# Performance work log

Hardware: AMD Instinct MI355X
Metric: run time of the kernel (lower is better)

The kernel has to match this reference:

```python
import jax, jax.numpy as jnp
import numpy as np

B, C, H, W = 16, 64, 64, 64
C1, C2 = 8, 32  # block_channels_1 = C/8, block_channels_2 = C/2


def _conv1x1(x, w, b):
    # x: [B,C,H,W], w: [O,C] (1x1 kernel), b: [O]
    return jnp.einsum('bchw,oc->bohw', x, w) + b[None, :, None, None]


def _maxpool2(x):
    # MaxPool2d(kernel_size=2): window 2x2, stride 2, no padding
    return jax.lax.reduce_window(x, -jnp.inf, jax.lax.max,
                                 (1, 1, 2, 2), (1, 1, 2, 2), 'VALID')


def setup_inputs() -> dict:
    key = jax.random.key(0)
    ks = jax.random.split(key, 10)
    s = lambda fan_in: 1.0 / np.sqrt(fan_in)
    return {
        'nonlocal_input': jax.random.normal(ks[0], (B, C, H, W), jnp.float32),
        # spectral-normalized conv weights are treated as the effective (already
        # normalized) weights; 1x1 kernels stored as [out, in]
        'w_delta': jax.random.normal(ks[1], (C1, C), jnp.float32) * s(C),
        'b_delta': jax.random.normal(ks[2], (C1,), jnp.float32) * 0.01,
        'w_phi': jax.random.normal(ks[3], (C1, C), jnp.float32) * s(C),
        'b_phi': jax.random.normal(ks[4], (C1,), jnp.float32) * 0.01,
        'w_g': jax.random.normal(ks[5], (C2, C), jnp.float32) * s(C),
        'b_g': jax.random.normal(ks[6], (C2,), jnp.float32) * 0.01,
        'w_last': jax.random.normal(ks[7], (C, C2), jnp.float32) * s(C2),
        'b_last': jax.random.normal(ks[8], (C,), jnp.float32) * 0.01,
        # torch init is zeros; use a nonzero value so the attention path matters
        'gamma': jnp.asarray([0.7], jnp.float32),
    }


def reference(nonlocal_input, w_delta, b_delta, w_phi, b_phi, w_g, b_g,
              w_last, b_last, gamma):
    x = nonlocal_input
    b, c, h, w = x.shape

    # delta: [B,C1,H,W] -> [B, HW, C1]
    delta = _conv1x1(x, w_delta, b_delta)
    delta = jnp.transpose(delta, (0, 2, 3, 1)).reshape(b, h * w, C1)

    # phi: conv + pool -> [B,C1,H/2,W/2]; NOTE: the original permutes
    # (1,0,2,3) BEFORE reshaping to [B, C1, HW/4] (faithful to source).
    phi = _maxpool2(_conv1x1(x, w_phi, b_phi))
    phi = jnp.transpose(phi, (1, 0, 2, 3)).reshape(b, C1, -1)

    # attention: [B, HW, HW/4]
    attn = jax.nn.softmax(jnp.einsum('bnk,bkm->bnm', delta, phi), axis=-1)

    # g: conv + pool -> [B, HW/4, C2]
    g = _maxpool2(_conv1x1(x, w_g, b_g))
    g = jnp.transpose(g, (0, 2, 3, 1)).reshape(b, -1, C2)

    out = jnp.einsum('bnm,bmc->bnc', attn, g)          # [B, HW, C2]
    out = out.reshape(b, h, w, C2).transpose(0, 3, 1, 2)  # [B, C2, H, W]

    return gamma[0] * _conv1x1(out, w_last, b_last) + x
```

## Files before the change

### kernel.cpp

```cpp
#include <hip/hip_runtime.h>
#include <hip/hip_bf16.h>
#include <math.h>

typedef __attribute__((ext_vector_type(8))) short bf16x8;
typedef __attribute__((ext_vector_type(4))) float f32x4;

#define B_   16
#define C_   64
#define C1_  8
#define C2_  32
#define HW_  4096
#define M_   1024
#define LOG2E 1.4426950408889634f
#define MFMA_BF16 __builtin_amdgcn_mfma_f32_16x16x32_bf16

__device__ __forceinline__ unsigned short f2bf(float f) {
  union { float f; unsigned u; } v; v.f = f;
  unsigned r = (v.u + 0x7fffu + ((v.u >> 16) & 1u)) >> 16;
  return (unsigned short)r;
}
__device__ __forceinline__ float bf2f(unsigned short h) {
  union { unsigned u; float f; } v; v.u = ((unsigned)h) << 16;
  return v.f;
}

__global__ __launch_bounds__(256, 4)
void k_pre(const float* __restrict__ x,
           const float* __restrict__ w_delta, const float* __restrict__ b_delta,
           const float* __restrict__ w_phi,  const float* __restrict__ b_phi,
           const float* __restrict__ w_g,    const float* __restrict__ b_g,
           unsigned short* __restrict__ delta_s,
           unsigned short* __restrict__ phi_s,
           unsigned short* __restrict__ g_t) {
  __shared__ float wd_s[C_*C1_];
  __shared__ float wp_s[C_*C1_];
  __shared__ float wg_s[C_*C2_];
  __shared__ float comb[2*64*49];
  int tid = threadIdx.x;
  for (int i = tid; i < C1_*C_; i += 256) {
    int o = i >> 6, c = i & 63;
    wd_s[c*C1_ + o] = w_delta[i];
    wp_s[c*C1_ + o] = w_phi[i];
  }
  for (int i = tid; i < C2_*C_; i += 256) {
    int o = i >> 6, c = i & 63;
    wg_s[c*C2_ + o] = w_g[i];
  }
  __syncthreads();

  int qt  = tid >> 6;
  int sub = tid & 63;
  int id  = blockIdx.x * 64 + sub;
  int pix = id & 3;
  int pm  = id >> 2;
  int b = pm >> 10;
  int m = pm & 1023;
  int py = 2*(m >> 5) + (pix >> 1);
  int px = 2*(m & 31) + (pix & 1);
  int n = py * 64 + px;

  const float* xp = x + ((size_t)b*C_ + qt*16)*HW_ + n;
  float xv[16];
  #pragma unroll
  for (int i = 0; i < 16; ++i) xv[i] = xp[(size_t)i * HW_];

  float ad[8], ap[8], ag[32];
  #pragma unroll
  for (int o = 0; o < 8; ++o) { ad[o] = 0.f; ap[o] = 0.f; }
  #pragma unroll
  for (int o = 0; o < 32; ++o) ag[o] = 0.f;

  int c0 = qt * 16;
  #pragma unroll
  for (int i = 0; i < 16; ++i) {
    int c = c0 + i;
    float v = xv[i];
    #pragma unroll
    for (int t = 0; t < 2; ++t) {
      float4 w = ((const float4*)(wd_s + c*C1_))[t];
      ad[4*t+0] += v*w.x; ad[4*t+1] += v*w.y; ad[4*t+2] += v*w.z; ad[4*t+3] += v*w.w;
    }
    #pragma unroll
    for (int t = 0; t < 2; ++t) {
      float4 w = ((const float4*)(wp_s + c*C1_))[t];
      ap[4*t+0] += v*w.x; ap[4*t+1] += v*w.y; ap[4*t+2] += v*w.z; ap[4*t+3] += v*w.w;
    }
    #pragma unroll
    for (int t = 0; t < 8; ++t) {
      float4 w = ((const float4*)(wg_s + c*C2_))[t];
      ag[4*t+0] += v*w.x; ag[4*t+1] += v*w.y; ag[4*t+2] += v*w.z; ag[4*t+3] += v*w.w;
    }
  }

  if (qt == 1 || qt == 3) {
    float* cb = comb + (((qt >> 1)*64) + sub)*49;
    #pragma unroll
    for (int o = 0; o < 8; ++o) { cb[o] = ad[o]; cb[8+o] = ap[o]; }
    #pragma unroll
    for (int o = 0; o < 32; ++o) cb[16+o] = ag[o];
  }
  __syncthreads();
  if (qt == 0 || qt == 2) {
    const float* cb = comb + (((qt >> 1)*64) + sub)*49;
    #pragma unroll
    for (int o = 0; o < 8; ++o) { ad[o] += cb[o]; ap[o] += cb[8+o]; }
    #pragma unroll
    for (int o = 0; o < 32; ++o) ag[o] += cb[16+o];
  }
  __syncthreads();
  if (qt == 2) {
    float* cb = comb + sub*49;
    #pragma unroll
    for (int o = 0; o < 8; ++o) { cb[o] = ad[o]; cb[8+o] = ap[o]; }
    #pragma unroll
    for (int o = 0; o < 32; ++o) cb[16+o] = ag[o];
  }
  __syncthreads();
  if (qt == 0) {
    const float* cb = comb + sub*49;
    #pragma unroll
    for (int o = 0; o < 8; ++o) { ad[o] += cb[o]; ap[o] += cb[8+o]; }
    #pragma unroll
    for (int o = 0; o < 32; ++o) ag[o] += cb[16+o];

    __align__(16) unsigned short row[16];
    #pragma unroll
    for (int o = 0; o < 8; ++o) {
      float v = (ad[o] + b_delta[o]) * LOG2E;
      unsigned short hi = f2bf(v);
      row[o]   = hi;
      row[8+o] = f2bf(v - bf2f(hi));
    }
    uint4* dst = (uint4*)(delta_s + ((size_t)b*HW_ + n)*16);
    dst[0] = *(uint4*)&row[0];
    dst[1] = *(uint4*)&row[8];

    #pragma unroll
    for (int o = 0; o < 8; ++o) {
      float v = ap[o];
      v = fmaxf(v, __shfl_xor(v, 1));
      v = fmaxf(v, __shfl_xor(v, 2));
      ap[o] = v;
    }
    #pragma unroll
    for (int o = 0; o < 32; ++o) {
      float v = ag[o];
      v = fmaxf(v, __shfl_xor(v, 1));
      v = fmaxf(v, __shfl_xor(v, 2));
      ag[o] = v;
    }

    if ((sub & 3) == 0) {
      #pragma unroll
      for (int cp = 0; cp < 8; ++cp) {
        int f = cp*16 + b;
        float v = ap[cp] + b_phi[cp];
        unsigned short hi = f2bf(v);
        unsigned short* pr = phi_s + ((size_t)(f >> 3)*M_ + m)*16;
        pr[f & 7]       = hi;
        pr[8 + (f & 7)] = f2bf(v - bf2f(hi));
      }
      #pragma unroll
      for (int o = 0; o < 32; ++o)
        g_t[((size_t)b*C2_ + o)*M_ + m] = f2bf(ag[o] + b_g[o]);
    }
  }
}

__global__ __launch_bounds__(256, 4)
void k_attn(const float* __restrict__ x,
            const unsigned short* __restrict__ delta_s,
            const unsigned short* __restrict__ phi_s,
            const unsigned short* __restrict__ g_t,
            const float* __restrict__ w_last,
            const float* __restrict__ b_last,
            const float* __restrict__ gamma,
            float* __restrict__ out) {
  __shared__ float cmb[2*32*40];
  __shared__ float o_sh[64*33];
  int tid  = threadIdx.x;
  int lane = tid & 63;
  int wv   = tid >> 6;
  int rg   = wv & 1;
  int kh   = wv >> 1;
  int r    = lane & 15;
  int q    = lane >> 4;
  int bx = blockIdx.x;
  int b  = bx >> 6;
  int n0 = (bx & 63) * 64;
  int row0 = n0 + rg*32;

  bf16x8 dfrag0 = *(const bf16x8*)(delta_s + ((size_t)b*HW_ + row0 + r)*16      + (q & 1)*8);
  bf16x8 dfrag1 = *(const bf16x8*)(delta_s + ((size_t)b*HW_ + row0 + 16 + r)*16 + (q & 1)*8);

  const unsigned short* phib = phi_s + (size_t)b*M_*16;
  const unsigned short* gb0  = g_t + ((size_t)b*C2_ + r)      * M_;
  const unsigned short* gb1  = g_t + ((size_t)b*C2_ + 16 + r) * M_;
  int phi_off = (q >> 1) * 8;
  int key0 = (r >> 2)*8 + (r & 3);
  int key1 = key0 + 4;

  bf16x8 ones;
  #pragma unroll
  for (int i = 0; i < 8; ++i) ones[i] = (short)0x3F80;

  f32x4 acc00 = {0,0,0,0}, acc01 = {0,0,0,0};
  f32x4 acc10 = {0,0,0,0}, acc11 = {0,0,0,0};
  f32x4 accd0 = {0,0,0,0}, accd1 = {0,0,0,0};
  f32x4 zero  = {0,0,0,0};

  int kbase = kh * 512;
  #pragma unroll 4
  for (int kc = 0; kc < 512; kc += 32) {
    int k0 = kbase + kc;
    bf16x8 aphi0 = *(const bf16x8*)(phib + (size_t)(k0 + key0)*16 + phi_off);
    bf16x8 aphi1 = *(const bf16x8*)(phib + (size_t)(k0 + key1)*16 + phi_off);
    bf16x8 bg0   = *(const bf16x8*)(gb0 + k0 + q*8);
    bf16x8 bg1   = *(const bf16x8*)(gb1 + k0 + q*8);

    f32x4 s0 = MFMA_BF16(aphi0, dfrag0, zero, 0, 0, 0);
    f32x4 s1 = MFMA_BF16(aphi1, dfrag0, zero, 0, 0, 0);
    union { bf16x8 v; __hip_bfloat162 h[4]; } e0;
    e0.h[0] = __float22bfloat162_rn(make_float2(__builtin_amdgcn_exp2f(s0[0]),
                                                __builtin_amdgcn_exp2f(s0[1])));
    e0.h[1] = __float22bfloat162_rn(make_float2(__builtin_amdgcn_exp2f(s0[2]),
                                                __builtin_amdgcn_exp2f(s0[3])));
    e0.h[2] = __float22bfloat162_rn(make_float2(__builtin_amdgcn_exp2f(s1[0]),
                                                __builtin_amdgcn_exp2f(s1[1])));
    e0.h[3] = __float22bfloat162_rn(make_float2(__builtin_amdgcn_exp2f(s1[2]),
                                                __builtin_amdgcn_exp2f(s1[3])));
    acc00 = MFMA_BF16(e0.v, bg0, acc00, 0, 0, 0);
    acc01 = MFMA_BF16(e0.v, bg1, acc01, 0, 0, 0);
    accd0 = MFMA_BF16(e0.v, ones, accd0, 0, 0, 0);

    f32x4 t0 = MFMA_BF16(aphi0, dfrag1, zero, 0, 0, 0);
    f32x4 t1 = MFMA_BF16(aphi1, dfrag1, zero, 0, 0, 0);
    union { bf16x8 v; __hip_bfloat162 h[4]; } e1;
    e1.h[0] = __float22bfloat162_rn(make_float2(__builtin_amdgcn_exp2f(t0[0]),
                                                __builtin_amdgcn_exp2f(t0[1])));
    e1.h[1] = __float22bfloat162_rn(make_float2(__builtin_amdgcn_exp2f(t0[2]),
                                                __builtin_amdgcn_exp2f(t0[3])));
    e1.h[2] = __float22bfloat162_rn(make_float2(__builtin_amdgcn_exp2f(t1[0]),
                                                __builtin_amdgcn_exp2f(t1[1])));
    e1.h[3] = __float22bfloat162_rn(make_float2(__builtin_amdgcn_exp2f(t1[2]),
                                                __builtin_amdgcn_exp2f(t1[3])));
    acc10 = MFMA_BF16(e1.v, bg0, acc10, 0, 0, 0);
    acc11 = MFMA_BF16(e1.v, bg1, acc11, 0, 0, 0);
    accd1 = MFMA_BF16(e1.v, ones, accd1, 0, 0, 0);
  }

  if (kh == 1) {
    float* cb = cmb + rg*32*40;
    #pragma unroll
    for (int reg = 0; reg < 4; ++reg) {
      int lr = q*4 + reg;
      cb[lr*40 + r]           = acc00[reg];
      cb[lr*40 + 16 + r]      = acc01[reg];
      cb[(16+lr)*40 + r]      = acc10[reg];
      cb[(16+lr)*40 + 16 + r] = acc11[reg];
      if (r == 0) {
        cb[lr*40 + 32]      = accd0[reg];
        cb[(16+lr)*40 + 32] = accd1[reg];
      }
    }
  }
  __syncthreads();
  if (kh == 0) {
    const float* cb = cmb + rg*32*40;
    #pragma unroll
    for (int reg = 0; reg < 4; ++reg) {
      int lr = q*4 + reg;
      float den0 = accd0[reg] + cb[lr*40 + 32];
      float den1 = accd1[reg] + cb[(16+lr)*40 + 32];
      float i0 = __builtin_amdgcn_rcpf(den0);
      float i1 = __builtin_amdgcn_rcpf(den1);
      o_sh[(rg*32 + lr)*33 + r]           = (acc00[reg] + cb[lr*40 + r])           * i0;
      o_sh[(rg*32 + lr)*33 + 16 + r]      = (acc01[reg] + cb[lr*40 + 16 + r])      * i0;
      o_sh[(rg*32 + 16 + lr)*33 + r]      = (acc10[reg] + cb[(16+lr)*40 + r])      * i1;
      o_sh[(rg*32 + 16 + lr)*33 + 16 + r] = (acc11[reg] + cb[(16+lr)*40 + 16 + r]) * i1;
    }
  }
  __syncthreads();

  int rr = tid & 63;
  int wq = tid >> 6;
  float o_reg[32];
  #pragma unroll
  for (int c = 0; c < 32; ++c) o_reg[c] = o_sh[rr*33 + c];
  float gm = gamma[0];
  for (int i = 0; i < 16; ++i) {
    int co = wq*16 + i;
    float a = b_last[co];
    #pragma unroll
    for (int c = 0; c < 32; ++c) a += w_last[co*32 + c] * o_reg[c];
    size_t oi = ((size_t)b*C_ + co)*HW_ + (size_t)(n0 + rr);
    out[oi] = gm * a + x[oi];
  }
}

extern "C" void kernel_launch(void* const* d_in, const int* in_sizes, int n_in,
                              void* d_out, int out_size, void* d_ws, size_t ws_size,
                              hipStream_t stream) {
  const float* x       = (const float*)d_in[0];
  const float* w_delta = (const float*)d_in[1];
  const float* b_delta = (const float*)d_in[2];
  const float* w_phi   = (const float*)d_in[3];
  const float* b_phi   = (const float*)d_in[4];
  const float* w_g     = (const float*)d_in[5];
  const float* b_g     = (const float*)d_in[6];
  const float* w_last  = (const float*)d_in[7];
  const float* b_last  = (const float*)d_in[8];
  const float* gamma   = (const float*)d_in[9];
  float* out = (float*)d_out;

  unsigned short* ws = (unsigned short*)d_ws;
  unsigned short* delta_s = ws;
  unsigned short* phi_s   = ws + (size_t)B_*HW_*16;
  unsigned short* g_t     = phi_s + (size_t)B_*M_*16;

  hipLaunchKernelGGL(k_pre, dim3(1024), dim3(256), 0, stream,
                     x, w_delta, b_delta, w_phi, b_phi, w_g, b_g,
                     delta_s, phi_s, g_t);
  hipLaunchKernelGGL(k_attn, dim3(1024), dim3(256), 0, stream,
                     x, delta_s, phi_s, g_t, w_last, b_last, gamma, out);
}
```

Before: 135.1 us.

## Split attention keys four ways per block and drop shared weight staging in pre kernel

The attention kernel now has each of its four waves cover all 64 query rows over a quarter of the key range. Previously waves were split two-by-two over row groups and key halves. This lets each loaded phi and g fragment feed four row tiles instead of two, cutting global load traffic per MFMA, at the cost of more accumulator registers and a three-way LDS reduction. The pre kernel also stops staging conv weights in shared memory with a barrier and reads them directly from global memory, relying on cache and scalar loads.

```diff
diff --git a/kernel.cpp b/kernel.cpp
--- a/kernel.cpp
+++ b/kernel.cpp
@@ -32,21 +32,8 @@
            unsigned short* __restrict__ delta_s,
            unsigned short* __restrict__ phi_s,
            unsigned short* __restrict__ g_t) {
-  __shared__ float wd_s[C_*C1_];
-  __shared__ float wp_s[C_*C1_];
-  __shared__ float wg_s[C_*C2_];
   __shared__ float comb[2*64*49];
   int tid = threadIdx.x;
-  for (int i = tid; i < C1_*C_; i += 256) {
-    int o = i >> 6, c = i & 63;
-    wd_s[c*C1_ + o] = w_delta[i];
-    wp_s[c*C1_ + o] = w_phi[i];
-  }
-  for (int i = tid; i < C2_*C_; i += 256) {
-    int o = i >> 6, c = i & 63;
-    wg_s[c*C2_ + o] = w_g[i];
-  }
-  __syncthreads();
 
   int qt  = tid >> 6;
   int sub = tid & 63;
@@ -59,37 +46,29 @@
   int px = 2*(m & 31) + (pix & 1);
   int n = py * 64 + px;
 
-  const float* xp = x + ((size_t)b*C_ + qt*16)*HW_ + n;
+  int c0 = qt * 16;
+  const float* xp = x + ((size_t)b*C_ + c0)*HW_ + n;
   float xv[16];
   #pragma unroll
   for (int i = 0; i < 16; ++i) xv[i] = xp[(size_t)i * HW_];
 
   float ad[8], ap[8], ag[32];
   #pragma unroll
-  for (int o = 0; o < 8; ++o) { ad[o] = 0.f; ap[o] = 0.f; }
-  #pragma unroll
-  for (int o = 0; o < 32; ++o) ag[o] = 0.f;
-
-  int c0 = qt * 16;
-  #pragma unroll
-  for (int i = 0; i < 16; ++i) {
-    int c = c0 + i;
-    float v = xv[i];
-    #pragma unroll
-    for (int t = 0; t < 2; ++t) {
-      float4 w = ((const float4*)(wd_s + c*C1_))[t];
-      ad[4*t+0] += v*w.x; ad[4*t+1] += v*w.y; ad[4*t+2] += v*w.z; ad[4*t+3] += v*w.w;
-    }
-    #pragma unroll
-    for (int t = 0; t < 2; ++t) {
-      float4 w = ((const float4*)(wp_s + c*C1_))[t];
-      ap[4*t+0] += v*w.x; ap[4*t+1] += v*w.y; ap[4*t+2] += v*w.z; ap[4*t+3] += v*w.w;
-    }
-    #pragma unroll
-    for (int t = 0; t < 8; ++t) {
-      float4 w = ((const float4*)(wg_s + c*C2_))[t];
-      ag[4*t+0] += v*w.x; ag[4*t+1] += v*w.y; ag[4*t+2] += v*w.z; ag[4*t+3] += v*w.w;
-    }
+  for (int o = 0; o < 8; ++o) {
+    const float* wd = w_delta + o*C_ + c0;
+    const float* wp = w_phi   + o*C_ + c0;
+    float accd = 0.f, accp = 0.f;
+    #pragma unroll
+    for (int i = 0; i < 16; ++i) { accd += xv[i]*wd[i]; accp += xv[i]*wp[i]; }
+    ad[o] = accd; ap[o] = accp;
+  }
+  #pragma unroll
+  for (int o = 0; o < 32; ++o) {
+    const float* wg = w_g + o*C_ + c0;
+    float a = 0.f;
+    #pragma unroll
+    for (int i = 0; i < 16; ++i) a += xv[i]*wg[i];
+    ag[o] = a;
   }
 
   if (qt == 1 || qt == 3) {
@@ -176,22 +155,21 @@
             const float* __restrict__ b_last,
             const float* __restrict__ gamma,
             float* __restrict__ out) {
-  __shared__ float cmb[2*32*40];
+  __shared__ float cmb[3*64*37];
   __shared__ float o_sh[64*33];
   int tid  = threadIdx.x;
   int lane = tid & 63;
-  int wv   = tid >> 6;
-  int rg   = wv & 1;
-  int kh   = wv >> 1;
+  int kh   = tid >> 6;
   int r    = lane & 15;
   int q    = lane >> 4;
   int bx = blockIdx.x;
   int b  = bx >> 6;
   int n0 = (bx & 63) * 64;
-  int row0 = n0 + rg*32;
-
-  bf16x8 dfrag0 = *(const bf16x8*)(delta_s + ((size_t)b*HW_ + row0 + r)*16      + (q & 1)*8);
-  bf16x8 dfrag1 = *(const bf16x8*)(delta_s + ((size_t)b*HW_ + row0 + 16 + r)*16 + (q & 1)*8);
+
+  bf16x8 df[4];
+  #pragma unroll
+  for (int t = 0; t < 4; ++t)
+    df[t] = *(const bf16x8*)(delta_s + ((size_t)b*HW_ + n0 + t*16 + r)*16 + (q & 1)*8);
 
   const unsigned short* phib = phi_s + (size_t)b*M_*16;
   const unsigned short* gb0  = g_t + ((size_t)b*C2_ + r)      * M_;
@@ -204,80 +182,74 @@
   #pragma unroll
   for (int i = 0; i < 8; ++i) ones[i] = (short)0x3F80;
 
-  f32x4 acc00 = {0,0,0,0}, acc01 = {0,0,0,0};
-  f32x4 acc10 = {0,0,0,0}, acc11 = {0,0,0,0};
-  f32x4 accd0 = {0,0,0,0}, accd1 = {0,0,0,0};
-  f32x4 zero  = {0,0,0,0};
-
-  int kbase = kh * 512;
-  #pragma unroll 4
-  for (int kc = 0; kc < 512; kc += 32) {
+  f32x4 acc[4][2];
+  f32x4 den[4];
+  f32x4 zero = {0,0,0,0};
+  #pragma unroll
+  for (int t = 0; t < 4; ++t) { acc[t][0] = zero; acc[t][1] = zero; den[t] = zero; }
+
+  int kbase = kh * 256;
+  #pragma unroll 2
+  for (int kc = 0; kc < 256; kc += 32) {
     int k0 = kbase + kc;
     bf16x8 aphi0 = *(const bf16x8*)(phib + (size_t)(k0 + key0)*16 + phi_off);
     bf16x8 aphi1 = *(const bf16x8*)(phib + (size_t)(k0 + key1)*16 + phi_off);
     bf16x8 bg0   = *(const bf16x8*)(gb0 + k0 + q*8);
     bf16x8 bg1   = *(const bf16x8*)(gb1 + k0 + q*8);
 
-    f32x4 s0 = MFMA_BF16(aphi0, dfrag0, zero, 0, 0, 0);
-    f32x4 s1 = MFMA_BF16(aphi1, dfrag0, zero, 0, 0, 0);
-    union { bf16x8 v; __hip_bfloat162 h[4]; } e0;
-    e0.h[0] = __float22bfloat162_rn(make_float2(__builtin_amdgcn_exp2f(s0[0]),
-                                                __builtin_amdgcn_exp2f(s0[1])));
-    e0.h[1] = __float22bfloat162_rn(make_float2(__builtin_amdgcn_exp2f(s0[2]),
-                                                __builtin_amdgcn_exp2f(s0[3])));
-    e0.h[2] = __float22bfloat162_rn(make_float2(__builtin_amdgcn_exp2f(s1[0]),
-                                                __builtin_amdgcn_exp2f(s1[1])));
-    e0.h[3] = __float22bfloat162_rn(make_float2(__builtin_amdgcn_exp2f(s1[2]),
-                                                __builtin_amdgcn_exp2f(s1[3])));
-    acc00 = MFMA_BF16(e0.v, bg0, acc00, 0, 0, 0);
-    acc01 = MFMA_BF16(e0.v, bg1, acc01, 0, 0, 0);
-    accd0 = MFMA_BF16(e0.v, ones, accd0, 0, 0, 0);
-
-    f32x4 t0 = MFMA_BF16(aphi0, dfrag1, zero, 0, 0, 0);
-    f32x4 t1 = MFMA_BF16(aphi1, dfrag1, zero, 0, 0, 0);
-    union { bf16x8 v; __hip_bfloat162 h[4]; } e1;
-    e1.h[0] = __float22bfloat162_rn(make_float2(__builtin_amdgcn_exp2f(t0[0]),
-                                                __builtin_amdgcn_exp2f(t0[1])));
-    e1.h[1] = __float22bfloat162_rn(make_float2(__builtin_amdgcn_exp2f(t0[2]),
-                                                __builtin_amdgcn_exp2f(t0[3])));
-    e1.h[2] = __float22bfloat162_rn(make_float2(__builtin_amdgcn_exp2f(t1[0]),
-                                                __builtin_amdgcn_exp2f(t1[1])));
-    e1.h[3] = __float22bfloat162_rn(make_float2(__builtin_amdgcn_exp2f(t1[2]),
-                                                __builtin_amdgcn_exp2f(t1[3])));
-    acc10 = MFMA_BF16(e1.v, bg0, acc10, 0, 0, 0);
-    acc11 = MFMA_BF16(e1.v, bg1, acc11, 0, 0, 0);
-    accd1 = MFMA_BF16(e1.v, ones, accd1, 0, 0, 0);
-  }
-
-  if (kh == 1) {
-    float* cb = cmb + rg*32*40;
-    #pragma unroll
-    for (int reg = 0; reg < 4; ++reg) {
-      int lr = q*4 + reg;
-      cb[lr*40 + r]           = acc00[reg];
-      cb[lr*40 + 16 + r]      = acc01[reg];
-      cb[(16+lr)*40 + r]      = acc10[reg];
-      cb[(16+lr)*40 + 16 + r] = acc11[reg];
-      if (r == 0) {
-        cb[lr*40 + 32]      = accd0[reg];
-        cb[(16+lr)*40 + 32] = accd1[reg];
+    #pragma unroll
+    for (int t = 0; t < 4; ++t) {
+      f32x4 s0 = MFMA_BF16(aphi0, df[t], zero, 0, 0, 0);
+      f32x4 s1 = MFMA_BF16(aphi1, df[t], zero, 0, 0, 0);
+      union { bf16x8 v; __hip_bfloat162 h[4]; } e;
+      e.h[0] = __float22bfloat162_rn(make_float2(__builtin_amdgcn_exp2f(s0[0]),
+                                                 __builtin_amdgcn_exp2f(s0[1])));
+      e.h[1] = __float22bfloat162_rn(make_float2(__builtin_amdgcn_exp2f(s0[2]),
+                                                 __builtin_amdgcn_exp2f(s0[3])));
+      e.h[2] = __float22bfloat162_rn(make_float2(__builtin_amdgcn_exp2f(s1[0]),
+                                                 __builtin_amdgcn_exp2f(s1[1])));
+      e.h[3] = __float22bfloat162_rn(make_float2(__builtin_amdgcn_exp2f(s1[2]),
+                                                 __builtin_amdgcn_exp2f(s1[3])));
+      acc[t][0] = MFMA_BF16(e.v, bg0, acc[t][0], 0, 0, 0);
+      acc[t][1] = MFMA_BF16(e.v, bg1, acc[t][1], 0, 0, 0);
+      den[t]    = MFMA_BF16(e.v, ones, den[t], 0, 0, 0);
+    }
+  }
+
+  if (kh != 0) {
+    float* cb = cmb + (kh-1)*64*37;
+    #pragma unroll
+    for (int t = 0; t < 4; ++t) {
+      #pragma unroll
+      for (int reg = 0; reg < 4; ++reg) {
+        int lr = t*16 + q*4 + reg;
+        cb[lr*37 + r]      = acc[t][0][reg];
+        cb[lr*37 + 16 + r] = acc[t][1][reg];
+        if (r == 0) cb[lr*37 + 32] = den[t][reg];
       }
     }
   }
   __syncthreads();
   if (kh == 0) {
-    const float* cb = cmb + rg*32*40;
-    #pragma unroll
-    for (int reg = 0; reg < 4; ++reg) {
-      int lr = q*4 + reg;
-      float den0 = accd0[reg] + cb[lr*40 + 32];
-      float den1 = accd1[reg] + cb[(16+lr)*40 + 32];
-      float i0 = __builtin_amdgcn_rcpf(den0);
-      float i1 = __builtin_amdgcn_rcpf(den1);
-      o_sh[(rg*32 + lr)*33 + r]           = (acc00[reg] + cb[lr*40 + r])           * i0;
-      o_sh[(rg*32 + lr)*33 + 16 + r]      = (acc01[reg] + cb[lr*40 + 16 + r])      * i0;
-      o_sh[(rg*32 + 16 + lr)*33 + r]      = (acc10[reg] + cb[(16+lr)*40 + r])      * i1;
-      o_sh[(rg*32 + 16 + lr)*33 + 16 + r] = (acc11[reg] + cb[(16+lr)*40 + 16 + r]) * i1;
+    #pragma unroll
+    for (int t = 0; t < 4; ++t) {
+      #pragma unroll
+      for (int reg = 0; reg < 4; ++reg) {
+        int lr = t*16 + q*4 + reg;
+        float o0 = acc[t][0][reg];
+        float o1 = acc[t][1][reg];
+        float dn = den[t][reg];
+        #pragma unroll
+        for (int p = 0; p < 3; ++p) {
+          const float* cb = cmb + p*64*37;
+          o0 += cb[lr*37 + r];
+          o1 += cb[lr*37 + 16 + r];
+          dn += cb[lr*37 + 32];
+        }
+        float iv = __builtin_amdgcn_rcpf(dn);
+        o_sh[lr*33 + r]      = o0 * iv;
+        o_sh[lr*33 + 16 + r] = o1 * iv;
+      }
     }
   }
   __syncthreads();
```

After: 142.2 us. 1.05x slower.
